# Optimization experiments

Hardware: AMD Instinct MI355X
Metric: run time of the kernel (lower is better)

Reference implementation:

```python
import jax, jax.numpy as jnp
import numpy as np

N_NODES = 50000
N_EDGES = 800000
IN_DIM = 128
EDGE_DIM = 128
OUT_DIM = 128
N_AGG = 4          # mean, max, min, std
N_SCALE = 3        # identity, amplification, attenuation
AVG_D_LOG = float(np.log(17.0))  # log(avg_degree + 1), PNA avg_d['log']
EPS = 1e-5


def setup_inputs() -> dict:
    key = jax.random.key(0)
    ks = jax.random.split(key, 10)
    pre_in = 2 * IN_DIM + EDGE_DIM                      # pretrans input dim
    post_in = (N_AGG * N_SCALE + 1) * IN_DIM            # posttrans input dim
    return {
        "node_feat": jax.random.normal(ks[0], (N_NODES, IN_DIM), jnp.float32),
        "edge_feat": jax.random.normal(ks[1], (N_EDGES, EDGE_DIM), jnp.float32),
        "w_pre": jax.random.normal(ks[2], (pre_in, IN_DIM), jnp.float32) * (1.0 / np.sqrt(pre_in)),
        "b_pre": jnp.zeros((IN_DIM,), jnp.float32),
        "w_post1": jax.random.normal(ks[3], (post_in, OUT_DIM), jnp.float32) * (1.0 / np.sqrt(post_in)),
        "b_post1": jnp.zeros((OUT_DIM,), jnp.float32),
        "w_post2": jax.random.normal(ks[4], (OUT_DIM, OUT_DIM), jnp.float32) * (1.0 / np.sqrt(OUT_DIM)),
        "b_post2": jnp.zeros((OUT_DIM,), jnp.float32),
        "src": jax.random.randint(ks[5], (N_EDGES,), 0, N_NODES, jnp.int32),
        "dst": jax.random.randint(ks[6], (N_EDGES,), 0, N_NODES, jnp.int32),
    }


def reference(node_feat, edge_feat, w_pre, b_pre, w_post1, b_post1,
              w_post2, b_post2, src, dst):
    n = node_feat.shape[0]
    # --- pretrans over edges: MLP(cat[src_h, dst_h, edge_feat]) -> message ---
    z = jnp.concatenate([node_feat[src], node_feat[dst], edge_feat], axis=-1)  # [E, 2d+de]
    msg = jax.nn.relu(z @ w_pre + b_pre)                                       # [E, d]

    # --- multi-aggregator scatter-reduce per destination node ---
    ones = jnp.ones((msg.shape[0],), msg.dtype)
    deg = jax.ops.segment_sum(ones, dst, num_segments=n)                       # [N]
    d_safe = jnp.maximum(deg, 1.0)[:, None]
    has_nb = (deg > 0)[:, None]

    s1 = jax.ops.segment_sum(msg, dst, num_segments=n)
    s2 = jax.ops.segment_sum(msg * msg, dst, num_segments=n)
    a_mean = s1 / d_safe
    a_var = jax.nn.relu(s2 / d_safe - a_mean * a_mean)
    a_std = jnp.sqrt(a_var + EPS)
    a_max = jnp.where(has_nb, jax.ops.segment_max(msg, dst, num_segments=n), 0.0)
    a_min = jnp.where(has_nb, jax.ops.segment_min(msg, dst, num_segments=n), 0.0)
    agg = jnp.concatenate([a_mean, a_max, a_min, a_std], axis=-1)              # [N, 4d]

    # --- degree scalers: identity, amplification, attenuation ---
    logd = jnp.log(deg + 1.0)[:, None]
    amp = agg * (logd / AVG_D_LOG)
    att = agg * (AVG_D_LOG / jnp.maximum(logd, EPS))
    h = jnp.concatenate([node_feat, agg, amp, att], axis=-1)                   # [N, 13d]

    # --- posttrans MLP + residual ---
    h1 = jax.nn.relu(h @ w_post1 + b_post1)
    out = h1 @ w_post2 + b_post2 + node_feat                                   # residual (in_dim == out_dim)
    return out
```

## Files before the change

### kernel.cpp

```cpp
#include <hip/hip_runtime.h>
#include <math.h>

#define N_NODES 50000
#define N_EDGES 800000
#define D 128
#define AVG_D_LOG 2.833213344056216f
#define EPS 1e-5f

typedef __attribute__((ext_vector_type(8))) short bf16x8;
typedef __attribute__((ext_vector_type(4))) float f32x4;

__device__ __forceinline__ unsigned short f2bf(float x) {
    unsigned u = __float_as_uint(x);
    u += 0x7fffu + ((u >> 16) & 1u);
    return (unsigned short)(u >> 16);
}
__device__ __forceinline__ unsigned pk2bf(float a, float b) {
    return (unsigned)f2bf(a) | ((unsigned)f2bf(b) << 16);
}
__device__ __forceinline__ float bf2f(unsigned short u) {
    return __uint_as_float(((unsigned)u) << 16);
}

__global__ void k_init(int* hist, float* s1, float* s2, float* mx, float* mn) {
    size_t stride = (size_t)gridDim.x * blockDim.x;
    size_t i0 = (size_t)blockIdx.x * blockDim.x + threadIdx.x;
    const size_t ND4 = (size_t)N_NODES * D / 4;
    float4 z4 = {0.f, 0.f, 0.f, 0.f};
    int4 inf4 = {0x7f800000, 0x7f800000, 0x7f800000, 0x7f800000};
    for (size_t t = i0; t < ND4; t += stride) {
        ((float4*)s1)[t] = z4; ((float4*)s2)[t] = z4; ((float4*)mx)[t] = z4;
        ((int4*)mn)[t] = inf4;
    }
    for (size_t t = i0; t < N_NODES; t += stride) hist[t] = 0;
}

__global__ void k_prep(const float* __restrict__ wp, const float* __restrict__ w1,
                       const float* __restrict__ w2,
                       unsigned short* __restrict__ wpT, unsigned short* __restrict__ w1T,
                       unsigned short* __restrict__ w2T,
                       const int* __restrict__ dst, int* hist) {
    int b = blockIdx.x, t = threadIdx.x;
    if (b < 192) {
        int idx = b * 256 + t;
        int k = idx >> 7, c = idx & 127;
        wpT[(size_t)c * 384 + k] = f2bf(wp[idx]);
    } else if (b < 1024) {
        int idx = (b - 192) * 256 + t;
        int k = idx >> 7, c = idx & 127;
        w1T[(size_t)c * 1664 + k] = f2bf(w1[idx]);
    } else if (b < 1088) {
        int idx = (b - 1024) * 256 + t;
        int k = idx >> 7, c = idx & 127;
        w2T[(size_t)c * 128 + k] = f2bf(w2[idx]);
    } else {
        int e = (b - 1088) * 256 + t;
        if (e < N_EDGES) atomicAdd(&hist[dst[e]], 1);
    }
}

__global__ __launch_bounds__(1024) void k_scan(const int* __restrict__ hist, int* cursor) {
    __shared__ int part[1024];
    int t = threadIdx.x;
    const int chunk = (N_NODES + 1023) / 1024;
    int lo = t * chunk;
    int hi = lo + chunk; if (hi > N_NODES) hi = N_NODES;
    int s = 0;
    for (int i = lo; i < hi; ++i) s += hist[i];
    part[t] = s;
    __syncthreads();
    for (int off = 1; off < 1024; off <<= 1) {
        int v = (t >= off) ? part[t - off] : 0;
        __syncthreads();
        part[t] += v;
        __syncthreads();
    }
    int run = (t == 0) ? 0 : part[t - 1];
    for (int i = lo; i < hi; ++i) { cursor[i] = run; run += hist[i]; }
}

__global__ void k_scatter(const int* __restrict__ dst, int* cursor, int* perm) {
    int e = blockIdx.x * blockDim.x + threadIdx.x;
    if (e < N_EDGES) {
        int pos = atomicAdd(&cursor[dst[e]], 1);
        perm[pos] = e;
    }
}

#define PFN(NC, PW0, PW1, PW2, PW3, PZ0, PZ1, PZ2, PZ3) do { \
    { int g = t;       int c = g >> 3, j = g & 7;  PW0 = *(const uint4*)(wpT + (size_t)c * 384 + (NC) * 64 + j * 8); } \
    { int g = t + 256; int c = g >> 3, j = g & 7;  PW1 = *(const uint4*)(wpT + (size_t)c * 384 + (NC) * 64 + j * 8); } \
    { int g = t + 512; int c = g >> 3, j = g & 7;  PW2 = *(const uint4*)(wpT + (size_t)c * 384 + (NC) * 64 + j * 8); } \
    { int g = t + 768; int c = g >> 3, j = g & 7;  PW3 = *(const uint4*)(wpT + (size_t)c * 384 + (NC) * 64 + j * 8); } \
    { int g = t;       int e = g >> 4, q = g & 15; PZ0 = *(const float4*)(ZROW(NC, e) + (((NC) & 1) * 64) + q * 4); } \
    { int g = t + 256; int e = g >> 4, q = g & 15; PZ1 = *(const float4*)(ZROW(NC, e) + (((NC) & 1) * 64) + q * 4); } \
    { int g = t + 512; int e = g >> 4, q = g & 15; PZ2 = *(const float4*)(ZROW(NC, e) + (((NC) & 1) * 64) + q * 4); } \
    { int g = t + 768; int e = g >> 4, q = g & 15; PZ3 = *(const float4*)(ZROW(NC, e) + (((NC) & 1) * 64) + q * 4); } \
} while (0)
#define WRN(OFF, PW0, PW1, PW2, PW3, PZ0, PZ1, PZ2, PZ3) do { \
    { int g = t;       int c = g >> 3, j = g & 7;  *(uint4*)(smem + (OFF) + c * 128 + ((j * 16) ^ ((c & 7) << 4))) = PW0; } \
    { int g = t + 256; int c = g >> 3, j = g & 7;  *(uint4*)(smem + (OFF) + c * 128 + ((j * 16) ^ ((c & 7) << 4))) = PW1; } \
    { int g = t + 512; int c = g >> 3, j = g & 7;  *(uint4*)(smem + (OFF) + c * 128 + ((j * 16) ^ ((c & 7) << 4))) = PW2; } \
    { int g = t + 768; int c = g >> 3, j = g & 7;  *(uint4*)(smem + (OFF) + c * 128 + ((j * 16) ^ ((c & 7) << 4))) = PW3; } \
    { int g = t;       int e = g >> 4, q = g & 15; uint2 hv = { pk2bf(PZ0.x, PZ0.y), pk2bf(PZ0.z, PZ0.w) }; \
      *(uint2*)(smem + (OFF) + 16384 + e * 128 + ((q * 8) ^ ((e & 7) << 4))) = hv; } \
    { int g = t + 256; int e = g >> 4, q = g & 15; uint2 hv = { pk2bf(PZ1.x, PZ1.y), pk2bf(PZ1.z, PZ1.w) }; \
      *(uint2*)(smem + (OFF) + 16384 + e * 128 + ((q * 8) ^ ((e & 7) << 4))) = hv; } \
    { int g = t + 512; int e = g >> 4, q = g & 15; uint2 hv = { pk2bf(PZ2.x, PZ2.y), pk2bf(PZ2.z, PZ2.w) }; \
      *(uint2*)(smem + (OFF) + 16384 + e * 128 + ((q * 8) ^ ((e & 7) << 4))) = hv; } \
    { int g = t + 768; int e = g >> 4, q = g & 15; uint2 hv = { pk2bf(PZ3.x, PZ3.y), pk2bf(PZ3.z, PZ3.w) }; \
      *(uint2*)(smem + (OFF) + 16384 + e * 128 + ((q * 8) ^ ((e & 7) << 4))) = hv; } \
} while (0)
#define MMO(OFF) do { \
    _Pragma("unroll") \
    for (int ks = 0; ks < 2; ++ks) { \
        bf16x8 afr[2], bfr[4]; \
        int kb = ks * 64 + lg * 16; \
        _Pragma("unroll") \
        for (int cf = 0; cf < 2; ++cf) { \
            int c = w * 32 + cf * 16 + lr; \
            afr[cf] = *(const bf16x8*)(smem + (OFF) + c * 128 + (kb ^ ((c & 7) << 4))); \
        } \
        _Pragma("unroll") \
        for (int eb = 0; eb < 4; ++eb) { \
            int e = eb * 16 + lr; \
            bfr[eb] = *(const bf16x8*)(smem + (OFF) + 16384 + e * 128 + (kb ^ ((e & 7) << 4))); \
        } \
        _Pragma("unroll") \
        for (int cf = 0; cf < 2; ++cf) \
            _Pragma("unroll") \
            for (int eb = 0; eb < 4; ++eb) \
                acc[cf][eb] = __builtin_amdgcn_mfma_f32_16x16x32_bf16( \
                    afr[cf], bfr[eb], acc[cf][eb], 0, 0, 0); \
    } \
} while (0)

__global__ __launch_bounds__(256) void k_pretrans_g(
    const float* __restrict__ nf, const float* __restrict__ ef,
    const unsigned short* __restrict__ wpT, const float* __restrict__ bp,
    const int* __restrict__ src, const int* __restrict__ dst,
    const int* __restrict__ perm,
    unsigned short* __restrict__ msgG)
{
    __shared__ __align__(16) char smem[24576];
    __shared__ int pidx[64], sidx[64], didx[64];
    __shared__ float sb[128];

    int t = threadIdx.x;
    int e0 = blockIdx.x * 64;
    if (t < 64) {
        int pe = perm[e0 + t];
        pidx[t] = pe; sidx[t] = src[pe]; didx[t] = dst[pe];
    }
    if (t < 128) sb[t] = bp[t];
    __syncthreads();

    int w  = t >> 6;
    int l  = t & 63;
    int lr = l & 15;
    int lg = l >> 4;

    f32x4 acc[2][4];
    #pragma unroll
    for (int i = 0; i < 2; ++i)
        #pragma unroll
        for (int j = 0; j < 4; ++j) acc[i][j] = (f32x4){0.f, 0.f, 0.f, 0.f};

    uint4  pw0, pw1, pw2, pw3;
    float4 pz0, pz1, pz2, pz3;

#define ZROW(NC, e) ((NC) < 2 ? nf + (size_t)sidx[e] * D : \
                     (NC) < 4 ? nf + (size_t)didx[e] * D : \
                                ef + (size_t)pidx[e] * D)
    PFN(0, pw0, pw1, pw2, pw3, pz0, pz1, pz2, pz3);
    WRN(0, pw0, pw1, pw2, pw3, pz0, pz1, pz2, pz3); PFN(1, pw0, pw1, pw2, pw3, pz0, pz1, pz2, pz3); __syncthreads(); MMO(0); __syncthreads();
    WRN(0, pw0, pw1, pw2, pw3, pz0, pz1, pz2, pz3); PFN(2, pw0, pw1, pw2, pw3, pz0, pz1, pz2, pz3); __syncthreads(); MMO(0); __syncthreads();
    WRN(0, pw0, pw1, pw2, pw3, pz0, pz1, pz2, pz3); PFN(3, pw0, pw1, pw2, pw3, pz0, pz1, pz2, pz3); __syncthreads(); MMO(0); __syncthreads();
    WRN(0, pw0, pw1, pw2, pw3, pz0, pz1, pz2, pz3); PFN(4, pw0, pw1, pw2, pw3, pz0, pz1, pz2, pz3); __syncthreads(); MMO(0); __syncthreads();
    WRN(0, pw0, pw1, pw2, pw3, pz0, pz1, pz2, pz3); PFN(5, pw0, pw1, pw2, pw3, pz0, pz1, pz2, pz3); __syncthreads(); MMO(0); __syncthreads();
    WRN(0, pw0, pw1, pw2, pw3, pz0, pz1, pz2, pz3);                                                 __syncthreads(); MMO(0); __syncthreads();
#undef ZROW

    #pragma unroll
    for (int cf = 0; cf < 2; ++cf)
        #pragma unroll
        for (int eb = 0; eb < 4; ++eb) {
            int e  = eb * 16 + lr;
            int c0 = w * 32 + cf * 16 + lg * 4;
            float v0 = fmaxf(acc[cf][eb][0] + sb[c0 + 0], 0.f);
            float v1 = fmaxf(acc[cf][eb][1] + sb[c0 + 1], 0.f);
            float v2 = fmaxf(acc[cf][eb][2] + sb[c0 + 2], 0.f);
            float v3 = fmaxf(acc[cf][eb][3] + sb[c0 + 3], 0.f);
            uint2 mv = { pk2bf(v0, v1), pk2bf(v2, v3) };
            *(uint2*)(smem + e * 256 + ((c0 * 2) ^ ((e & 7) << 4))) = mv;
        }
    __syncthreads();
    #pragma unroll
    for (int p = 0; p < 4; ++p) {
        int e = (t >> 4) + p * 16;
        int q = t & 15;
        uint4 v = *(const uint4*)(smem + e * 256 + q * 16);
        int qq = q ^ (e & 7);
        *(uint4*)(msgG + (size_t)(e0 + e) * D + qq * 8) = v;
    }
}

__global__ __launch_bounds__(256) void k_agg(
    const unsigned short* __restrict__ msgG,
    const int* __restrict__ cursor, const int* __restrict__ hist,
    float* __restrict__ s1, float* __restrict__ s2,
    float* __restrict__ mx, float* __restrict__ mn, float* __restrict__ scal)
{
    int t = threadIdx.x;
    int n = blockIdx.x * 4 + (t >> 6);
    int tl = t & 63;
    int deg = hist[n];
    int re  = cursor[n];
    int rs  = re - deg;

    float sum0 = 0.f, sum1 = 0.f, sq0 = 0.f, sq1 = 0.f;
    float mx0 = -3.402823e38f, mx1 = -3.402823e38f;
    float mn0 =  3.402823e38f, mn1 =  3.402823e38f;
    const uint* mg = (const uint*)msgG;
    for (int e = 0; e < deg; ++e) {
        uint v = mg[(size_t)(rs + e) * 64 + tl];
        float a = bf2f((unsigned short)(v & 0xffff));
        float b = bf2f((unsigned short)(v >> 16));
        sum0 += a; sum1 += b; sq0 += a * a; sq1 += b * b;
        mx0 = fmaxf(mx0, a); mx1 = fmaxf(mx1, b);
        mn0 = fminf(mn0, a); mn1 = fminf(mn1, b);
    }
    float dg = (float)deg;
    float ds = fmaxf(dg, 1.f);
    bool nb = deg > 0;
    float m0 = sum0 / ds, m1 = sum1 / ds;
    float sd0 = sqrtf(fmaxf(sq0 / ds - m0 * m0, 0.f) + EPS);
    float sd1 = sqrtf(fmaxf(sq1 / ds - m1 * m1, 0.f) + EPS);
    size_t base = (size_t)n * D + tl * 2;
    *(float2*)&s1[base] = (float2){m0, m1};
    *(float2*)&s2[base] = (float2){sd0, sd1};
    *(float2*)&mx[base] = (float2){nb ? mx0 : 0.f, nb ? mx1 : 0.f};
    *(float2*)&mn[base] = (float2){nb ? mn0 : 0.f, nb ? mn1 : 0.f};
    if (tl == 0) {
        float logd = logf(dg + 1.f);
        scal[2 * n]     = logd / AVG_D_LOG;
        scal[2 * n + 1] = AVG_D_LOG / fmaxf(logd, EPS);
    }
}

__global__ __launch_bounds__(256) void k_pretrans(
    const float* __restrict__ nf, const float* __restrict__ ef,
    const unsigned short* __restrict__ wpT, const float* __restrict__ bp,
    const int* __restrict__ src, const int* __restrict__ dst,
    const int* __restrict__ perm,
    float* s1, float* s2, float* mx, float* mn)
{
    __shared__ __align__(16) char smem[24576];
    __shared__ int pidx[64], sidx[64], didx[64];
    __shared__ int seg_start[65], seg_dst[64];
    __shared__ int nseg_s;
    __shared__ float sb[128];

    int t = threadIdx.x;
    int e0 = blockIdx.x * 64;
    if (t < 64) {
        int pe = perm[e0 + t];
        pidx[t] = pe; sidx[t] = src[pe]; didx[t] = dst[pe];
    }
    if (t < 128) sb[t] = bp[t];
    __syncthreads();

    int w  = t >> 6;
    int l  = t & 63;
    int lr = l & 15;
    int lg = l >> 4;

    f32x4 acc[2][4];
    #pragma unroll
    for (int i = 0; i < 2; ++i)
        #pragma unroll
        for (int j = 0; j < 4; ++j) acc[i][j] = (f32x4){0.f, 0.f, 0.f, 0.f};

    uint4  pw0, pw1, pw2, pw3;
    float4 pz0, pz1, pz2, pz3;

#define ZROW(NC, e) ((NC) < 2 ? nf + (size_t)sidx[e] * D : \
                     (NC) < 4 ? nf + (size_t)didx[e] * D : \
                                ef + (size_t)pidx[e] * D)
    PFN(0, pw0, pw1, pw2, pw3, pz0, pz1, pz2, pz3);
    WRN(0, pw0, pw1, pw2, pw3, pz0, pz1, pz2, pz3); PFN(1, pw0, pw1, pw2, pw3, pz0, pz1, pz2, pz3); __syncthreads(); MMO(0); __syncthreads();
    WRN(0, pw0, pw1, pw2, pw3, pz0, pz1, pz2, pz3); PFN(2, pw0, pw1, pw2, pw3, pz0, pz1, pz2, pz3); __syncthreads(); MMO(0); __syncthreads();
    WRN(0, pw0, pw1, pw2, pw3, pz0, pz1, pz2, pz3); PFN(3, pw0, pw1, pw2, pw3, pz0, pz1, pz2, pz3); __syncthreads(); MMO(0); __syncthreads();
    WRN(0, pw0, pw1, pw2, pw3, pz0, pz1, pz2, pz3); PFN(4, pw0, pw1, pw2, pw3, pz0, pz1, pz2, pz3); __syncthreads(); MMO(0); __syncthreads();
    WRN(0, pw0, pw1, pw2, pw3, pz0, pz1, pz2, pz3); PFN(5, pw0, pw1, pw2, pw3, pz0, pz1, pz2, pz3); __syncthreads(); MMO(0); __syncthreads();
    WRN(0, pw0, pw1, pw2, pw3, pz0, pz1, pz2, pz3);                                                 __syncthreads(); MMO(0); __syncthreads();
#undef ZROW

    #pragma unroll
    for (int cf = 0; cf < 2; ++cf)
        #pragma unroll
        for (int eb = 0; eb < 4; ++eb) {
            int e  = eb * 16 + lr;
            int c0 = w * 32 + cf * 16 + lg * 4;
            float v0 = fmaxf(acc[cf][eb][0] + sb[c0 + 0], 0.f);
            float v1 = fmaxf(acc[cf][eb][1] + sb[c0 + 1], 0.f);
            float v2 = fmaxf(acc[cf][eb][2] + sb[c0 + 2], 0.f);
            float v3 = fmaxf(acc[cf][eb][3] + sb[c0 + 3], 0.f);
            uint2 mv = { pk2bf(v0, v1), pk2bf(v2, v3) };
            *(uint2*)(smem + e * 256 + ((c0 * 2) ^ ((e & 7) << 4))) = mv;
        }
    if (t == 0) {
        int ns = 0;
        for (int e = 0; e < 64; ++e) {
            if (e == 0 || didx[e] != didx[e - 1]) { seg_dst[ns] = didx[e]; seg_start[ns] = e; ++ns; }
        }
        seg_start[ns] = 64; nseg_s = ns;
    }
    __syncthreads();
    int nseg = nseg_s;
    for (int idx = t; idx < nseg * D; idx += 256) {
        int sg = idx >> 7, c = idx & 127;
        int eb2 = seg_start[sg], ee = seg_start[sg + 1];
        float s = 0.f, q = 0.f, vmax = 0.f, vmin = __int_as_float(0x7f800000);
        for (int e = eb2; e < ee; ++e) {
            float v = bf2f(*(const unsigned short*)(smem + e * 256 + ((c * 2) ^ ((e & 7) << 4))));
            s += v; q += v * v;
            vmax = fmaxf(vmax, v); vmin = fminf(vmin, v);
        }
        size_t base = (size_t)seg_dst[sg] * D + c;
        atomicAdd(&s1[base], s);
        atomicAdd(&s2[base], q);
        atomicMax((int*)&mx[base], __float_as_int(vmax));
        atomicMin((int*)&mn[base], __float_as_int(vmin));
    }
}

#undef PFN
#undef WRN
#undef MMO

__global__ void k_finalize(float* s1, float* s2, float* mx, float* mn,
                           const int* __restrict__ hist, float* scal) {
    size_t idx = (size_t)blockIdx.x * blockDim.x + threadIdx.x;
    if (idx >= (size_t)N_NODES * D) return;
    int n = (int)(idx >> 7);
    int c = (int)(idx & 127);
    float dg = (float)hist[n];
    float ds = fmaxf(dg, 1.f);
    float m  = s1[idx] / ds;
    float var = fmaxf(s2[idx] / ds - m * m, 0.f);
    float sd  = sqrtf(var + EPS);
    bool nb = dg > 0.f;
    s1[idx] = m;
    mx[idx] = nb ? mx[idx] : 0.f;
    mn[idx] = nb ? mn[idx] : 0.f;
    s2[idx] = sd;
    if (c == 0) {
        float logd = logf(dg + 1.f);
        scal[2 * n]     = logd / AVG_D_LOG;
        scal[2 * n + 1] = AVG_D_LOG / fmaxf(logd, EPS);
    }
}

__global__ __launch_bounds__(256, 3) void k_post(
    const float* __restrict__ nf,
    const float* __restrict__ amean, const float* __restrict__ amax,
    const float* __restrict__ amin,  const float* __restrict__ astd,
    const float* __restrict__ scal,
    const unsigned short* __restrict__ w1T, const float* __restrict__ b1,
    const unsigned short* __restrict__ w2T, const float* __restrict__ b2,
    float* __restrict__ out)
{
    __shared__ __align__(16) char smem[49152];
    __shared__ float samp[64], satt[64], sb1[128], sb2[128];

    int t = threadIdx.x;
    int n0 = blockIdx.x * 64;
    if (t < 64) {
        int n = n0 + t;
        samp[t] = (n < N_NODES) ? scal[2 * n] : 0.f;
        satt[t] = (n < N_NODES) ? scal[2 * n + 1] : 0.f;
    }
    if (t < 128) { sb1[t] = b1[t]; sb2[t] = b2[t]; }
    __syncthreads();

    int w  = t >> 6, l = t & 63, lr = l & 15, lg = l >> 4;
    f32x4 acc[2][4];
    #pragma unroll
    for (int i = 0; i < 2; ++i)
        #pragma unroll
        for (int j = 0; j < 4; ++j) acc[i][j] = (f32x4){0.f, 0.f, 0.f, 0.f};

    for (int chunk = 0; chunk < 13; ++chunk) {
        #pragma unroll
        for (int p = 0; p < 8; ++p) {
            int g = t + 256 * p;
            int c = g >> 4, j = g & 15;
            uint4 wv = *(const uint4*)(w1T + (size_t)c * 1664 + chunk * 128 + j * 8);
            *(uint4*)(smem + c * 256 + ((j * 16) ^ ((c & 7) << 4))) = wv;
        }
        const float* base;
        int r;
        if (chunk == 0) { base = nf; r = 0; }
        else {
            int b = (chunk - 1) & 3;
            r = (chunk - 1) >> 2;
            base = (b == 0) ? amean : (b == 1) ? amax : (b == 2) ? amin : astd;
        }
        #pragma unroll
        for (int p = 0; p < 8; ++p) {
            int g = t + 256 * p;
            int e = g >> 5, q = g & 31;
            int n = n0 + e;
            float4 fv = {0.f, 0.f, 0.f, 0.f};
            if (n < N_NODES) {
                fv = *(const float4*)(base + (size_t)n * D + q * 4);
                if (r == 1) { float sc = samp[e]; fv.x *= sc; fv.y *= sc; fv.z *= sc; fv.w *= sc; }
                else if (r == 2) { float sc = satt[e]; fv.x *= sc; fv.y *= sc; fv.z *= sc; fv.w *= sc; }
            }
            uint2 hv = { pk2bf(fv.x, fv.y), pk2bf(fv.z, fv.w) };
            *(uint2*)(smem + 32768 + e * 256 + ((q * 8) ^ ((e & 7) << 4))) = hv;
        }
        __syncthreads();
        #pragma unroll
        for (int ks = 0; ks < 4; ++ks) {
            bf16x8 afr[2], bfr[4];
            int kb = ks * 64 + lg * 16;
            #pragma unroll
            for (int cf = 0; cf < 2; ++cf) {
                int c = w * 32 + cf * 16 + lr;
                afr[cf] = *(const bf16x8*)(smem + c * 256 + (kb ^ ((c & 7) << 4)));
            }
            #pragma unroll
            for (int eb = 0; eb < 4; ++eb) {
                int e = eb * 16 + lr;
                bfr[eb] = *(const bf16x8*)(smem + 32768 + e * 256 + (kb ^ ((e & 7) << 4)));
            }
            #pragma unroll
            for (int cf = 0; cf < 2; ++cf)
                #pragma unroll
                for (int eb = 0; eb < 4; ++eb)
                    acc[cf][eb] = __builtin_amdgcn_mfma_f32_16x16x32_bf16(
                        afr[cf], bfr[eb], acc[cf][eb], 0, 0, 0);
        }
        __syncthreads();
    }

    #pragma unroll
    for (int cf = 0; cf < 2; ++cf)
        #pragma unroll
        for (int eb = 0; eb < 4; ++eb) {
            int e  = eb * 16 + lr;
            int c0 = w * 32 + cf * 16 + lg * 4;
            float v0 = fmaxf(acc[cf][eb][0] + sb1[c0 + 0], 0.f);
            float v1 = fmaxf(acc[cf][eb][1] + sb1[c0 + 1], 0.f);
            float v2 = fmaxf(acc[cf][eb][2] + sb1[c0 + 2], 0.f);
            float v3 = fmaxf(acc[cf][eb][3] + sb1[c0 + 3], 0.f);
            uint2 hv = { pk2bf(v0, v1), pk2bf(v2, v3) };
            *(uint2*)(smem + 32768 + e * 256 + ((c0 * 2) ^ ((e & 7) << 4))) = hv;
        }
    #pragma unroll
    for (int p = 0; p < 8; ++p) {
        int g = t + 256 * p;
        int c = g >> 4, j = g & 15;
        uint4 wv = *(const uint4*)(w2T + (size_t)c * 128 + j * 8);
        *(uint4*)(smem + c * 256 + ((j * 16) ^ ((c & 7) << 4))) = wv;
    }
    __syncthreads();

    f32x4 acc2[2][4];
    #pragma unroll
    for (int i = 0; i < 2; ++i)
        #pragma unroll
        for (int j = 0; j < 4; ++j) acc2[i][j] = (f32x4){0.f, 0.f, 0.f, 0.f};
    #pragma unroll
    for (int ks = 0; ks < 4; ++ks) {
        bf16x8 afr[2], bfr[4];
        int kb = ks * 64 + lg * 16;
        #pragma unroll
        for (int cf = 0; cf < 2; ++cf) {
            int c = w * 32 + cf * 16 + lr;
            afr[cf] = *(const bf16x8*)(smem + c * 256 + (kb ^ ((c & 7) << 4)));
        }
        #pragma unroll
        for (int eb = 0; eb < 4; ++eb) {
            int e = eb * 16 + lr;
            bfr[eb] = *(const bf16x8*)(smem + 32768 + e * 256 + (kb ^ ((e & 7) << 4)));
        }
        #pragma unroll
        for (int cf = 0; cf < 2; ++cf)
            #pragma unroll
            for (int eb = 0; eb < 4; ++eb)
                acc2[cf][eb] = __builtin_amdgcn_mfma_f32_16x16x32_bf16(
                    afr[cf], bfr[eb], acc2[cf][eb], 0, 0, 0);
    }

    #pragma unroll
    for (int cf = 0; cf < 2; ++cf)
        #pragma unroll
        for (int eb = 0; eb < 4; ++eb) {
            int n = n0 + eb * 16 + lr;
            if (n < N_NODES) {
                int c0 = w * 32 + cf * 16 + lg * 4;
                float4 rv = *(const float4*)(nf + (size_t)n * D + c0);
                float4 ov = { acc2[cf][eb][0] + sb2[c0 + 0] + rv.x,
                              acc2[cf][eb][1] + sb2[c0 + 1] + rv.y,
                              acc2[cf][eb][2] + sb2[c0 + 2] + rv.z,
                              acc2[cf][eb][3] + sb2[c0 + 3] + rv.w };
                *(float4*)(out + (size_t)n * D + c0) = ov;
            }
        }
}

extern "C" void kernel_launch(void* const* d_in, const int* in_sizes, int n_in,
                              void* d_out, int out_size, void* d_ws, size_t ws_size,
                              hipStream_t stream) {
    const float* nf = (const float*)d_in[0];
    const float* ef = (const float*)d_in[1];
    const float* wp = (const float*)d_in[2];
    const float* bp = (const float*)d_in[3];
    const float* w1 = (const float*)d_in[4];
    const float* b1 = (const float*)d_in[5];
    const float* w2 = (const float*)d_in[6];
    const float* b2 = (const float*)d_in[7];
    const int* src  = (const int*)d_in[8];
    const int* dst  = (const int*)d_in[9];
    float* out = (float*)d_out;

    const size_t ND = (size_t)N_NODES * D;
    const size_t MSG_SH = (size_t)N_EDGES * D;
    char* wsb = (char*)d_ws;
    int*   hist   = (int*)wsb;
    int*   cursor = hist + 50048;
    int*   perm   = cursor + 50048;
    unsigned short* wpT = (unsigned short*)(perm + N_EDGES);
    unsigned short* w1T = wpT + 49152;
    unsigned short* w2T = w1T + 212992;
    unsigned short* tail = w2T + 16384;

    unsigned short* msgG = tail;
    float* s1   = (float*)(msgG + MSG_SH);
    float* s2   = s1 + ND;
    float* mx   = s2 + ND;
    float* mn   = mx + ND;
    float* scal = mn + ND;
    size_t need_csr = (size_t)((char*)(scal + 100096) - wsb);

    bool use_csr = ws_size >= need_csr;
    if (!use_csr) {
        s1   = (float*)tail;
        s2   = s1 + ND;
        mx   = s2 + ND;
        mn   = mx + ND;
        scal = mn + ND;
    }

    if (use_csr) {
        hipMemsetAsync(hist, 0, N_NODES * sizeof(int), stream);
    } else {
        hipLaunchKernelGGL(k_init, dim3(2048), dim3(256), 0, stream, hist, s1, s2, mx, mn);
    }
    hipLaunchKernelGGL(k_prep, dim3(1088 + (N_EDGES + 255) / 256), dim3(256), 0, stream,
                       wp, w1, w2, wpT, w1T, w2T, dst, hist);
    hipLaunchKernelGGL(k_scan, dim3(1), dim3(1024), 0, stream, hist, cursor);
    hipLaunchKernelGGL(k_scatter, dim3((N_EDGES + 255) / 256), dim3(256), 0, stream, dst, cursor, perm);
    if (use_csr) {
        hipLaunchKernelGGL(k_pretrans_g, dim3(N_EDGES / 64), dim3(256), 0, stream,
                           nf, ef, wpT, bp, src, dst, perm, msgG);
        hipLaunchKernelGGL(k_agg, dim3(N_NODES / 4), dim3(256), 0, stream,
                           msgG, cursor, hist, s1, s2, mx, mn, scal);
    } else {
        hipLaunchKernelGGL(k_pretrans, dim3(N_EDGES / 64), dim3(256), 0, stream,
                           nf, ef, wpT, bp, src, dst, perm, s1, s2, mx, mn);
        hipLaunchKernelGGL(k_finalize, dim3((unsigned)((ND + 255) / 256)), dim3(256), 0, stream,
                           s1, s2, mx, mn, hist, scal);
    }
    hipLaunchKernelGGL(k_post, dim3((N_NODES + 63) / 64), dim3(256), 0, stream,
                       nf, s1, mx, mn, s2, scal, w1T, b1, w2T, b2, out);
}
```

Before: 585.7 us.

## Precompute per-node pretrans projections and gather them per edge

The edge MLP's src and dst parts are split off: a new node kernel computes nf@W_src and nf@W_dst+bias once per node (stored as bf16). The edge kernel then only multiplies edge features and adds the two gathered projections. This cuts the per-edge GEMM work to a third and replaces gathers of fp32 node rows with gathers of bf16 projections. Edges are now processed in original order, so the aggregation kernel reads messages indirectly through perm, which gives up the contiguous CSR reads. The projections are rounded to bf16 before the add, which adds a little rounding error.

```diff
diff --git a/kernel.cpp b/kernel.cpp
--- a/kernel.cpp
+++ b/kernel.cpp
@@ -84,6 +84,230 @@
     if (e < N_EDGES) {
         int pos = atomicAdd(&cursor[dst[e]], 1);
         perm[pos] = e;
+    }
+}
+
+#define MM256(ACC, AOFF, BOFF) do { \
+    _Pragma("unroll") \
+    for (int ks = 0; ks < 4; ++ks) { \
+        bf16x8 afr[2], bfr[4]; \
+        int kb = ks * 64 + lg * 16; \
+        _Pragma("unroll") \
+        for (int cf = 0; cf < 2; ++cf) { \
+            int c = w * 32 + cf * 16 + lr; \
+            afr[cf] = *(const bf16x8*)(smem + (AOFF) + c * 256 + (kb ^ ((c & 7) << 4))); \
+        } \
+        _Pragma("unroll") \
+        for (int eb = 0; eb < 4; ++eb) { \
+            int e = eb * 16 + lr; \
+            bfr[eb] = *(const bf16x8*)(smem + (BOFF) + e * 256 + (kb ^ ((e & 7) << 4))); \
+        } \
+        _Pragma("unroll") \
+        for (int cf = 0; cf < 2; ++cf) \
+            _Pragma("unroll") \
+            for (int eb = 0; eb < 4; ++eb) \
+                ACC[cf][eb] = __builtin_amdgcn_mfma_f32_16x16x32_bf16( \
+                    afr[cf], bfr[eb], ACC[cf][eb], 0, 0, 0); \
+    } \
+} while (0)
+
+__global__ __launch_bounds__(256) void k_node(
+    const float* __restrict__ nf, const unsigned short* __restrict__ wpT,
+    const float* __restrict__ bp,
+    unsigned short* __restrict__ p1, unsigned short* __restrict__ p2)
+{
+    __shared__ __align__(16) char smem[49152];
+    __shared__ float sb[128];
+    int t = threadIdx.x;
+    int n0 = blockIdx.x * 64;
+    if (t < 128) sb[t] = bp[t];
+    int w = t >> 6, l = t & 63, lr = l & 15, lg = l >> 4;
+
+    f32x4 acc1[2][4], acc2[2][4];
+    #pragma unroll
+    for (int i = 0; i < 2; ++i)
+        #pragma unroll
+        for (int j = 0; j < 4; ++j) { acc1[i][j] = (f32x4){0.f,0.f,0.f,0.f}; acc2[i][j] = (f32x4){0.f,0.f,0.f,0.f}; }
+
+    #pragma unroll
+    for (int p = 0; p < 8; ++p) {
+        int g = t + 256 * p;
+        int e = g >> 5, q = g & 31;
+        int n = n0 + e;
+        float4 fv = {0.f, 0.f, 0.f, 0.f};
+        if (n < N_NODES) fv = *(const float4*)(nf + (size_t)n * D + q * 4);
+        uint2 hv = { pk2bf(fv.x, fv.y), pk2bf(fv.z, fv.w) };
+        *(uint2*)(smem + 32768 + e * 256 + ((q * 8) ^ ((e & 7) << 4))) = hv;
+    }
+    #pragma unroll
+    for (int p = 0; p < 8; ++p) {
+        int g = t + 256 * p;
+        int c = g >> 4, j = g & 15;
+        uint4 wv = *(const uint4*)(wpT + (size_t)c * 384 + j * 8);
+        *(uint4*)(smem + c * 256 + ((j * 16) ^ ((c & 7) << 4))) = wv;
+    }
+    __syncthreads();
+    MM256(acc1, 0, 32768);
+    __syncthreads();
+    #pragma unroll
+    for (int p = 0; p < 8; ++p) {
+        int g = t + 256 * p;
+        int c = g >> 4, j = g & 15;
+        uint4 wv = *(const uint4*)(wpT + (size_t)c * 384 + 128 + j * 8);
+        *(uint4*)(smem + c * 256 + ((j * 16) ^ ((c & 7) << 4))) = wv;
+    }
+    __syncthreads();
+    MM256(acc2, 0, 32768);
+    __syncthreads();
+
+    #pragma unroll
+    for (int cf = 0; cf < 2; ++cf)
+        #pragma unroll
+        for (int eb = 0; eb < 4; ++eb) {
+            int e  = eb * 16 + lr;
+            int c0 = w * 32 + cf * 16 + lg * 4;
+            uint2 v1 = { pk2bf(acc1[cf][eb][0], acc1[cf][eb][1]),
+                         pk2bf(acc1[cf][eb][2], acc1[cf][eb][3]) };
+            *(uint2*)(smem + e * 256 + ((c0 * 2) ^ ((e & 7) << 4))) = v1;
+            uint2 v2 = { pk2bf(acc2[cf][eb][0] + sb[c0 + 0], acc2[cf][eb][1] + sb[c0 + 1]),
+                         pk2bf(acc2[cf][eb][2] + sb[c0 + 2], acc2[cf][eb][3] + sb[c0 + 3]) };
+            *(uint2*)(smem + 16384 + e * 256 + ((c0 * 2) ^ ((e & 7) << 4))) = v2;
+        }
+    __syncthreads();
+    #pragma unroll
+    for (int p = 0; p < 4; ++p) {
+        int e = (t >> 4) + p * 16;
+        int q = t & 15;
+        int n = n0 + e;
+        if (n < N_NODES) {
+            int qq = q ^ (e & 7);
+            uint4 v1 = *(const uint4*)(smem + e * 256 + q * 16);
+            *(uint4*)(p1 + (size_t)n * D + qq * 8) = v1;
+            uint4 v2 = *(const uint4*)(smem + 16384 + e * 256 + q * 16);
+            *(uint4*)(p2 + (size_t)n * D + qq * 8) = v2;
+        }
+    }
+}
+
+__global__ __launch_bounds__(256) void k_edge(
+    const float* __restrict__ ef, const unsigned short* __restrict__ wpT,
+    const int* __restrict__ src, const int* __restrict__ dst,
+    const unsigned short* __restrict__ p1, const unsigned short* __restrict__ p2,
+    unsigned short* __restrict__ msgG)
+{
+    __shared__ __align__(16) char smem[49152];
+    __shared__ int sidx[64], didx[64];
+
+    int t = threadIdx.x;
+    int e0 = blockIdx.x * 64;
+    if (t < 64) { sidx[t] = src[e0 + t]; didx[t] = dst[e0 + t]; }
+    int w = t >> 6, l = t & 63, lr = l & 15, lg = l >> 4;
+
+    f32x4 acc[2][4];
+    #pragma unroll
+    for (int i = 0; i < 2; ++i)
+        #pragma unroll
+        for (int j = 0; j < 4; ++j) acc[i][j] = (f32x4){0.f, 0.f, 0.f, 0.f};
+
+    #pragma unroll
+    for (int p = 0; p < 8; ++p) {
+        int g = t + 256 * p;
+        int c = g >> 4, j = g & 15;
+        uint4 wv = *(const uint4*)(wpT + (size_t)c * 384 + 256 + j * 8);
+        *(uint4*)(smem + c * 256 + ((j * 16) ^ ((c & 7) << 4))) = wv;
+    }
+    #pragma unroll
+    for (int p = 0; p < 8; ++p) {
+        int g = t + 256 * p;
+        int e = g >> 5, q = g & 31;
+        float4 fv = *(const float4*)(ef + (size_t)(e0 + e) * D + q * 4);
+        uint2 hv = { pk2bf(fv.x, fv.y), pk2bf(fv.z, fv.w) };
+        *(uint2*)(smem + 32768 + e * 256 + ((q * 8) ^ ((e & 7) << 4))) = hv;
+    }
+    __syncthreads();
+    MM256(acc, 0, 32768);
+    __syncthreads();
+    #pragma unroll
+    for (int p = 0; p < 4; ++p) {
+        int g = t + 256 * p;
+        int e = g >> 4, q = g & 15;
+        uint4 v1 = *(const uint4*)(p1 + (size_t)sidx[e] * D + q * 8);
+        *(uint4*)(smem + e * 256 + ((q * 16) ^ ((e & 7) << 4))) = v1;
+        uint4 v2 = *(const uint4*)(p2 + (size_t)didx[e] * D + q * 8);
+        *(uint4*)(smem + 16384 + e * 256 + ((q * 16) ^ ((e & 7) << 4))) = v2;
+    }
+    __syncthreads();
+    #pragma unroll
+    for (int cf = 0; cf < 2; ++cf)
+        #pragma unroll
+        for (int eb = 0; eb < 4; ++eb) {
+            int e  = eb * 16 + lr;
+            int c0 = w * 32 + cf * 16 + lg * 4;
+            uint2 a1 = *(const uint2*)(smem + e * 256 + ((c0 * 2) ^ ((e & 7) << 4)));
+            uint2 a2 = *(const uint2*)(smem + 16384 + e * 256 + ((c0 * 2) ^ ((e & 7) << 4)));
+            float v0 = acc[cf][eb][0] + bf2f((unsigned short)(a1.x & 0xffff)) + bf2f((unsigned short)(a2.x & 0xffff));
+            float v1 = acc[cf][eb][1] + bf2f((unsigned short)(a1.x >> 16))    + bf2f((unsigned short)(a2.x >> 16));
+            float v2 = acc[cf][eb][2] + bf2f((unsigned short)(a1.y & 0xffff)) + bf2f((unsigned short)(a2.y & 0xffff));
+            float v3 = acc[cf][eb][3] + bf2f((unsigned short)(a1.y >> 16))    + bf2f((unsigned short)(a2.y >> 16));
+            uint2 mv = { pk2bf(fmaxf(v0, 0.f), fmaxf(v1, 0.f)),
+                         pk2bf(fmaxf(v2, 0.f), fmaxf(v3, 0.f)) };
+            *(uint2*)(smem + 32768 + e * 256 + ((c0 * 2) ^ ((e & 7) << 4))) = mv;
+        }
+    __syncthreads();
+    #pragma unroll
+    for (int p = 0; p < 4; ++p) {
+        int e = (t >> 4) + p * 16;
+        int q = t & 15;
+        uint4 v = *(const uint4*)(smem + 32768 + e * 256 + q * 16);
+        int qq = q ^ (e & 7);
+        *(uint4*)(msgG + (size_t)(e0 + e) * D + qq * 8) = v;
+    }
+}
+
+__global__ __launch_bounds__(256) void k_agg(
+    const unsigned short* __restrict__ msgG,
+    const int* __restrict__ cursor, const int* __restrict__ hist,
+    const int* __restrict__ perm,
+    float* __restrict__ s1, float* __restrict__ s2,
+    float* __restrict__ mx, float* __restrict__ mn, float* __restrict__ scal)
+{
+    int t = threadIdx.x;
+    int n = blockIdx.x * 4 + (t >> 6);
+    int tl = t & 63;
+    int deg = hist[n];
+    int re  = cursor[n];
+    int rs  = re - deg;
+
+    float sum0 = 0.f, sum1 = 0.f, sq0 = 0.f, sq1 = 0.f;
+    float mx0 = -3.402823e38f, mx1 = -3.402823e38f;
+    float mn0 =  3.402823e38f, mn1 =  3.402823e38f;
+    const uint* mg = (const uint*)msgG;
+    int pe_next = (deg > 0) ? perm[rs] : 0;
+    for (int e = 0; e < deg; ++e) {
+        int pe = pe_next;
+        if (e + 1 < deg) pe_next = perm[rs + e + 1];
+        uint v = mg[(size_t)pe * 64 + tl];
+        float a = bf2f((unsigned short)(v & 0xffff));
+        float b = bf2f((unsigned short)(v >> 16));
+        sum0 += a; sum1 += b; sq0 += a * a; sq1 += b * b;
+        mx0 = fmaxf(mx0, a); mx1 = fmaxf(mx1, b);
+        mn0 = fminf(mn0, a); mn1 = fminf(mn1, b);
+    }
+    float dg = (float)deg;
+    float ds = fmaxf(dg, 1.f);
+    bool nb = deg > 0;
+    float m0 = sum0 / ds, m1 = sum1 / ds;
+    float sd0 = sqrtf(fmaxf(sq0 / ds - m0 * m0, 0.f) + EPS);
+    float sd1 = sqrtf(fmaxf(sq1 / ds - m1 * m1, 0.f) + EPS);
+    size_t base = (size_t)n * D + tl * 2;
+    *(float2*)&s1[base] = (float2){m0, m1};
+    *(float2*)&s2[base] = (float2){sd0, sd1};
+    *(float2*)&mx[base] = (float2){nb ? mx0 : 0.f, nb ? mx1 : 0.f};
+    *(float2*)&mn[base] = (float2){nb ? mn0 : 0.f, nb ? mn1 : 0.f};
+    if (tl == 0) {
+        float logd = logf(dg + 1.f);
+        scal[2 * n]     = logd / AVG_D_LOG;
+        scal[2 * n + 1] = AVG_D_LOG / fmaxf(logd, EPS);
     }
 }
 
@@ -135,119 +359,6 @@
     } \
 } while (0)
 
-__global__ __launch_bounds__(256) void k_pretrans_g(
-    const float* __restrict__ nf, const float* __restrict__ ef,
-    const unsigned short* __restrict__ wpT, const float* __restrict__ bp,
-    const int* __restrict__ src, const int* __restrict__ dst,
-    const int* __restrict__ perm,
-    unsigned short* __restrict__ msgG)
-{
-    __shared__ __align__(16) char smem[24576];
-    __shared__ int pidx[64], sidx[64], didx[64];
-    __shared__ float sb[128];
-
-    int t = threadIdx.x;
-    int e0 = blockIdx.x * 64;
-    if (t < 64) {
-        int pe = perm[e0 + t];
-        pidx[t] = pe; sidx[t] = src[pe]; didx[t] = dst[pe];
-    }
-    if (t < 128) sb[t] = bp[t];
-    __syncthreads();
-
-    int w  = t >> 6;
-    int l  = t & 63;
-    int lr = l & 15;
-    int lg = l >> 4;
-
-    f32x4 acc[2][4];
-    #pragma unroll
-    for (int i = 0; i < 2; ++i)
-        #pragma unroll
-        for (int j = 0; j < 4; ++j) acc[i][j] = (f32x4){0.f, 0.f, 0.f, 0.f};
-
-    uint4  pw0, pw1, pw2, pw3;
-    float4 pz0, pz1, pz2, pz3;
-
-#define ZROW(NC, e) ((NC) < 2 ? nf + (size_t)sidx[e] * D : \
-                     (NC) < 4 ? nf + (size_t)didx[e] * D : \
-                                ef + (size_t)pidx[e] * D)
-    PFN(0, pw0, pw1, pw2, pw3, pz0, pz1, pz2, pz3);
-    WRN(0, pw0, pw1, pw2, pw3, pz0, pz1, pz2, pz3); PFN(1, pw0, pw1, pw2, pw3, pz0, pz1, pz2, pz3); __syncthreads(); MMO(0); __syncthreads();
-    WRN(0, pw0, pw1, pw2, pw3, pz0, pz1, pz2, pz3); PFN(2, pw0, pw1, pw2, pw3, pz0, pz1, pz2, pz3); __syncthreads(); MMO(0); __syncthreads();
-    WRN(0, pw0, pw1, pw2, pw3, pz0, pz1, pz2, pz3); PFN(3, pw0, pw1, pw2, pw3, pz0, pz1, pz2, pz3); __syncthreads(); MMO(0); __syncthreads();
-    WRN(0, pw0, pw1, pw2, pw3, pz0, pz1, pz2, pz3); PFN(4, pw0, pw1, pw2, pw3, pz0, pz1, pz2, pz3); __syncthreads(); MMO(0); __syncthreads();
-    WRN(0, pw0, pw1, pw2, pw3, pz0, pz1, pz2, pz3); PFN(5, pw0, pw1, pw2, pw3, pz0, pz1, pz2, pz3); __syncthreads(); MMO(0); __syncthreads();
-    WRN(0, pw0, pw1, pw2, pw3, pz0, pz1, pz2, pz3);                                                 __syncthreads(); MMO(0); __syncthreads();
-#undef ZROW
-
-    #pragma unroll
-    for (int cf = 0; cf < 2; ++cf)
-        #pragma unroll
-        for (int eb = 0; eb < 4; ++eb) {
-            int e  = eb * 16 + lr;
-            int c0 = w * 32 + cf * 16 + lg * 4;
-            float v0 = fmaxf(acc[cf][eb][0] + sb[c0 + 0], 0.f);
-            float v1 = fmaxf(acc[cf][eb][1] + sb[c0 + 1], 0.f);
-            float v2 = fmaxf(acc[cf][eb][2] + sb[c0 + 2], 0.f);
-            float v3 = fmaxf(acc[cf][eb][3] + sb[c0 + 3], 0.f);
-            uint2 mv = { pk2bf(v0, v1), pk2bf(v2, v3) };
-            *(uint2*)(smem + e * 256 + ((c0 * 2) ^ ((e & 7) << 4))) = mv;
-        }
-    __syncthreads();
-    #pragma unroll
-    for (int p = 0; p < 4; ++p) {
-        int e = (t >> 4) + p * 16;
-        int q = t & 15;
-        uint4 v = *(const uint4*)(smem + e * 256 + q * 16);
-        int qq = q ^ (e & 7);
-        *(uint4*)(msgG + (size_t)(e0 + e) * D + qq * 8) = v;
-    }
-}
-
-__global__ __launch_bounds__(256) void k_agg(
-    const unsigned short* __restrict__ msgG,
-    const int* __restrict__ cursor, const int* __restrict__ hist,
-    float* __restrict__ s1, float* __restrict__ s2,
-    float* __restrict__ mx, float* __restrict__ mn, float* __restrict__ scal)
-{
-    int t = threadIdx.x;
-    int n = blockIdx.x * 4 + (t >> 6);
-    int tl = t & 63;
-    int deg = hist[n];
-    int re  = cursor[n];
-    int rs  = re - deg;
-
-    float sum0 = 0.f, sum1 = 0.f, sq0 = 0.f, sq1 = 0.f;
-    float mx0 = -3.402823e38f, mx1 = -3.402823e38f;
-    float mn0 =  3.402823e38f, mn1 =  3.402823e38f;
-    const uint* mg = (const uint*)msgG;
-    for (int e = 0; e < deg; ++e) {
-        uint v = mg[(size_t)(rs + e) * 64 + tl];
-        float a = bf2f((unsigned short)(v & 0xffff));
-        float b = bf2f((unsigned short)(v >> 16));
-        sum0 += a; sum1 += b; sq0 += a * a; sq1 += b * b;
-        mx0 = fmaxf(mx0, a); mx1 = fmaxf(mx1, b);
-        mn0 = fminf(mn0, a); mn1 = fminf(mn1, b);
-    }
-    float dg = (float)deg;
-    float ds = fmaxf(dg, 1.f);
-    bool nb = deg > 0;
-    float m0 = sum0 / ds, m1 = sum1 / ds;
-    float sd0 = sqrtf(fmaxf(sq0 / ds - m0 * m0, 0.f) + EPS);
-    float sd1 = sqrtf(fmaxf(sq1 / ds - m1 * m1, 0.f) + EPS);
-    size_t base = (size_t)n * D + tl * 2;
-    *(float2*)&s1[base] = (float2){m0, m1};
-    *(float2*)&s2[base] = (float2){sd0, sd1};
-    *(float2*)&mx[base] = (float2){nb ? mx0 : 0.f, nb ? mx1 : 0.f};
-    *(float2*)&mn[base] = (float2){nb ? mn0 : 0.f, nb ? mn1 : 0.f};
-    if (tl == 0) {
-        float logd = logf(dg + 1.f);
-        scal[2 * n]     = logd / AVG_D_LOG;
-        scal[2 * n + 1] = AVG_D_LOG / fmaxf(logd, EPS);
-    }
-}
-
 __global__ __launch_bounds__(256) void k_pretrans(
     const float* __restrict__ nf, const float* __restrict__ ef,
     const unsigned short* __restrict__ wpT, const float* __restrict__ bp,
@@ -422,27 +533,7 @@
             *(uint2*)(smem + 32768 + e * 256 + ((q * 8) ^ ((e & 7) << 4))) = hv;
         }
         __syncthreads();
-        #pragma unroll
-        for (int ks = 0; ks < 4; ++ks) {
-            bf16x8 afr[2], bfr[4];
-            int kb = ks * 64 + lg * 16;
-            #pragma unroll
-            for (int cf = 0; cf < 2; ++cf) {
-                int c = w * 32 + cf * 16 + lr;
-                afr[cf] = *(const bf16x8*)(smem + c * 256 + (kb ^ ((c & 7) << 4)));
-            }
-            #pragma unroll
-            for (int eb = 0; eb < 4; ++eb) {
-                int e = eb * 16 + lr;
-                bfr[eb] = *(const bf16x8*)(smem + 32768 + e * 256 + (kb ^ ((e & 7) << 4)));
-            }
-            #pragma unroll
-            for (int cf = 0; cf < 2; ++cf)
-                #pragma unroll
-                for (int eb = 0; eb < 4; ++eb)
-                    acc[cf][eb] = __builtin_amdgcn_mfma_f32_16x16x32_bf16(
-                        afr[cf], bfr[eb], acc[cf][eb], 0, 0, 0);
-        }
+        MM256(acc, 0, 32768);
         __syncthreads();
     }
 
@@ -473,27 +564,7 @@
     for (int i = 0; i < 2; ++i)
         #pragma unroll
         for (int j = 0; j < 4; ++j) acc2[i][j] = (f32x4){0.f, 0.f, 0.f, 0.f};
-    #pragma unroll
-    for (int ks = 0; ks < 4; ++ks) {
-        bf16x8 afr[2], bfr[4];
-        int kb = ks * 64 + lg * 16;
-        #pragma unroll
-        for (int cf = 0; cf < 2; ++cf) {
-            int c = w * 32 + cf * 16 + lr;
-            afr[cf] = *(const bf16x8*)(smem + c * 256 + (kb ^ ((c & 7) << 4)));
-        }
-        #pragma unroll
-        for (int eb = 0; eb < 4; ++eb) {
-            int e = eb * 16 + lr;
-            bfr[eb] = *(const bf16x8*)(smem + 32768 + e * 256 + (kb ^ ((e & 7) << 4)));
-        }
-        #pragma unroll
-        for (int cf = 0; cf < 2; ++cf)
-            #pragma unroll
-            for (int eb = 0; eb < 4; ++eb)
-                acc2[cf][eb] = __builtin_amdgcn_mfma_f32_16x16x32_bf16(
-                    afr[cf], bfr[eb], acc2[cf][eb], 0, 0, 0);
-    }
+    MM256(acc2, 0, 32768);
 
     #pragma unroll
     for (int cf = 0; cf < 2; ++cf)
@@ -538,7 +609,9 @@
     unsigned short* w2T = w1T + 212992;
     unsigned short* tail = w2T + 16384;
 
-    unsigned short* msgG = tail;
+    unsigned short* p1   = tail;
+    unsigned short* p2   = p1 + ND;
+    unsigned short* msgG = p2 + ND;
     float* s1   = (float*)(msgG + MSG_SH);
     float* s2   = s1 + ND;
     float* mx   = s2 + ND;
@@ -565,10 +638,12 @@
     hipLaunchKernelGGL(k_scan, dim3(1), dim3(1024), 0, stream, hist, cursor);
     hipLaunchKernelGGL(k_scatter, dim3((N_EDGES + 255) / 256), dim3(256), 0, stream, dst, cursor, perm);
     if (use_csr) {
-        hipLaunchKernelGGL(k_pretrans_g, dim3(N_EDGES / 64), dim3(256), 0, stream,
-                           nf, ef, wpT, bp, src, dst, perm, msgG);
+        hipLaunchKernelGGL(k_node, dim3((N_NODES + 63) / 64), dim3(256), 0, stream,
+                           nf, wpT, bp, p1, p2);
+        hipLaunchKernelGGL(k_edge, dim3(N_EDGES / 64), dim3(256), 0, stream,
+                           ef, wpT, src, dst, p1, p2, msgG);
         hipLaunchKernelGGL(k_agg, dim3(N_NODES / 4), dim3(256), 0, stream,
-                           msgG, cursor, hist, s1, s2, mx, mn, scal);
+                           msgG, cursor, hist, perm, s1, s2, mx, mn, scal);
     } else {
         hipLaunchKernelGGL(k_pretrans, dim3(N_EDGES / 64), dim3(256), 0, stream,
                            nf, ef, wpT, bp, src, dst, perm, s1, s2, mx, mn);
```

New measurement: 551.5 us. 5.8% less time.
